# Kernel tuning notes

Measured on AMD Instinct MI355X. Metric: run time of the kernel, lower is better.

The kernel has to match this reference:

```python
import jax, jax.numpy as jnp
import numpy as np

B, G, T, N = 2, 4, 64, 300
D = 256          # detr_dim == feature_dim
R = 4            # ffn_dim_ratio
MD = 32          # motion_dim


def _xavier(key, shape):
    lim = (6.0 / (shape[0] + shape[1])) ** 0.5
    return jax.random.uniform(key, shape, jnp.float32, -lim, lim)


def setup_inputs() -> dict:
    key = jax.random.key(0)
    ks = jax.random.split(key, 16)
    feats = jax.random.normal(ks[0], (B, G, T, N, D), jnp.float32)
    boxes = jax.random.uniform(ks[1], (B, G, T, N, 4), jnp.float32)
    masks = jax.random.bernoulli(ks[2], 0.3, (B, G, T, N))
    # per-trajectory permutation of frame ids 0..T-1 (unique -> unambiguous scatter)
    u = jax.random.uniform(ks[3], (B, G, N, T))
    times = jnp.swapaxes(jnp.argsort(u, axis=-1).astype(jnp.int32), 2, 3)  # [B,G,T,N]
    return {
        'trajectory_features': feats,
        'trajectory_boxes': boxes,
        'trajectory_masks': masks,
        'trajectory_times': times,
        'adp_w1': _xavier(ks[4], (D, D * R)), 'adp_b1': jnp.zeros((D * R,), jnp.float32),
        'adp_w2': _xavier(ks[5], (D * R, D)), 'adp_b2': jnp.zeros((D,), jnp.float32),
        'norm_g': jnp.ones((D,), jnp.float32), 'norm_b': jnp.zeros((D,), jnp.float32),
        'mot_w1': _xavier(ks[6], (12, MD // 2)), 'mot_b1': jnp.zeros((MD // 2,), jnp.float32),
        'mot_w2': _xavier(ks[7], (MD // 2, MD)), 'mot_b2': jnp.zeros((MD,), jnp.float32),
        'fus_w1': _xavier(ks[8], (D + MD, D)), 'fus_b1': jnp.zeros((D,), jnp.float32),
        'fus_w2': _xavier(ks[9], (D, D)), 'fus_b2': jnp.zeros((D,), jnp.float32),
        'ffn_w1': _xavier(ks[10], (D, D * R)), 'ffn_b1': jnp.zeros((D * R,), jnp.float32),
        'ffn_w2': _xavier(ks[11], (D * R, D)), 'ffn_b2': jnp.zeros((D,), jnp.float32),
        'fnorm_g': jnp.ones((D,), jnp.float32), 'fnorm_b': jnp.zeros((D,), jnp.float32),
    }


def _ffn(x, w1, b1, w2, b2):
    return jax.nn.gelu(x @ w1 + b1, approximate=False) @ w2 + b2


def _ln(x, g, b):
    m = x.mean(-1, keepdims=True)
    v = ((x - m) ** 2).mean(-1, keepdims=True)
    return (x - m) / jnp.sqrt(v + 1e-5) * g + b


def _motion_features(boxes, masks, times, mot_w1, mot_b1, mot_w2, mot_b2):
    # boxes [B,G,T,N,4] -> trajectory-major [B,G,N,T,*]
    b_, g_, t_, n_ = masks.shape
    md = mot_b2.shape[0]
    bx = jnp.swapaxes(boxes, 2, 3)              # [B,G,N,T,4]
    valid = ~jnp.swapaxes(masks, 2, 3)          # [B,G,N,T]
    tm = jnp.swapaxes(times, 2, 3)              # [B,G,N,T]
    # sort valid entries first, by time (stable)
    order = jnp.argsort(jnp.where(valid, tm, t_ + 1), axis=-1)
    sb = jnp.take_along_axis(bx, order[..., None], axis=3)   # sorted boxes
    st = jnp.take_along_axis(tm, order, axis=-1)             # sorted times
    cnt = valid.sum(-1)                                      # [B,G,N]
    pos = jnp.arange(t_)
    in_count = pos[None, None, None, :] < cnt[..., None]
    dt = jnp.maximum(st - jnp.roll(st, 1, axis=-1), 1).astype(sb.dtype)[..., None]
    mask_v = ((pos >= 1)[None, None, None, :] & in_count)[..., None]
    vel = jnp.where(mask_v, (sb - jnp.roll(sb, 1, axis=3)) / dt, 0.0)
    mask_a = ((pos >= 2)[None, None, None, :] & in_count)[..., None]
    acc = jnp.where(mask_a, (vel - jnp.roll(vel, 1, axis=3)) / dt, 0.0)
    mv = jnp.concatenate([sb, vel, acc], axis=-1)            # [B,G,N,T,12]
    enc = jax.nn.gelu(mv @ mot_w1 + mot_b1, approximate=False) @ mot_w2 + mot_b2
    write = in_count & (cnt >= 2)[..., None] & (st < t_)
    frame = jnp.where(write, st, t_)                         # t_ -> dropped
    bi, gi, ni, ti = jnp.meshgrid(jnp.arange(b_), jnp.arange(g_), jnp.arange(n_),
                                  jnp.arange(t_), indexing='ij')
    out = jnp.zeros((b_, g_, t_, n_, md), sb.dtype)
    return out.at[bi, gi, frame, ni].set(enc, mode='drop')


def reference(trajectory_features, trajectory_boxes, trajectory_masks, trajectory_times,
              adp_w1, adp_b1, adp_w2, adp_b2, norm_g, norm_b,
              mot_w1, mot_b1, mot_w2, mot_b2,
              fus_w1, fus_b1, fus_w2, fus_b2,
              ffn_w1, ffn_b1, ffn_w2, ffn_b2, fnorm_g, fnorm_b):
    x = trajectory_features + _ffn(trajectory_features, adp_w1, adp_b1, adp_w2, adp_b2)
    x = _ln(x, norm_g, norm_b)
    motion = _motion_features(trajectory_boxes, trajectory_masks, trajectory_times,
                              mot_w1, mot_b1, mot_w2, mot_b2)
    cat = jnp.concatenate([x, motion], axis=-1)
    fused = jax.nn.gelu(cat @ fus_w1 + fus_b1, approximate=False) @ fus_w2 + fus_b2
    fused = fused + _ffn(fused, ffn_w1, ffn_b1, ffn_w2, ffn_b2)
    fused = _ln(fused, fnorm_g, fnorm_b)
    return fused, motion
```

## Files before the change

kernel.cpp:

```cpp
#include <hip/hip_runtime.h>

typedef __bf16 bf16x8 __attribute__((ext_vector_type(8)));
typedef __bf16 bf16x4 __attribute__((ext_vector_type(4)));
typedef float f32x4 __attribute__((ext_vector_type(4)));

namespace {

constexpr int T_ = 64;
constexpr int N_ = 300;
constexpr int MD_ = 32;
constexpr int BG_ = 8;
constexpr long MROWS_ = (long)BG_ * T_ * N_;
constexpr long FUSED_N = MROWS_ * 256;
constexpr int MB = 64;

constexpr long PA1 = 0;
constexpr long PA2 = 262144;
constexpr long PF1 = 524288;
constexpr long PF2 = 598016;
constexpr long PN1 = 663552;
constexpr long PN2 = 925696;

__device__ __forceinline__ float gelu_f(float x) {
  const float x2 = x * x;
  const float z2 = x * fmaf(x2, 0.07135481627f, 1.5957691216f);
  const float t = __builtin_amdgcn_rcpf(1.0f + __expf(z2));
  return x * (1.0f - t);
}

__device__ __forceinline__ float gelu_exact(float x) {
  return 0.5f * x * (1.0f + erff(x * 0.7071067811865476f));
}

__global__ void k_zero_flag(int* f) { *f = 0; }

__global__ void k_detect_mask(const unsigned char* __restrict__ m, int nbytes,
                              int* __restrict__ f) {
  int i = blockIdx.x * 256 + threadIdx.x;
  if (i < nbytes && (i & 3) != 0 && m[i] != 0) atomicOr(f, 1);
}

__global__ __launch_bounds__(256)
void k_motion(const float* __restrict__ boxes, const void* __restrict__ masks,
              const int* __restrict__ times,
              const float* __restrict__ mw1, const float* __restrict__ mb1,
              const float* __restrict__ mw2, const float* __restrict__ mb2,
              float* __restrict__ motion, const int* __restrict__ flagp) {
  __shared__ int slot[4][T_];
  __shared__ int sts[4][T_];
  __shared__ float sbx[4][T_][4];
  __shared__ float otile[4][T_][MD_];
  const int tid = threadIdx.x;
  const int w = tid >> 6, l = tid & 63;
  const int traj = blockIdx.x * 4 + w;
  const int bg = traj / N_, n = traj - bg * N_;
  const int isbool = *flagp;
  const long idx = ((long)bg * T_ + l) * N_ + n;
  const bool msk = isbool ? (((const unsigned char*)masks)[idx] != 0)
                          : (((const int*)masks)[idx] != 0);
  const bool valid = !msk;
  const int tm = times[idx];

  slot[w][l] = -1;
  sts[w][l] = 0;
  *(float4*)&sbx[w][l][0] = make_float4(0.f, 0.f, 0.f, 0.f);
  __syncthreads();
  if (valid) slot[w][tm] = l;
  __syncthreads();

  const int ot = slot[w][l];
  const bool vp = ot >= 0;
  const unsigned long long bal = __ballot(vp);
  const int cnt = __builtin_popcountll(bal);
  const int pos = __builtin_popcountll(bal & ((1ull << l) - 1ull));
  if (vp) {
    sts[w][pos] = l;
    const float4 bx = *(const float4*)(boxes + (((long)bg * T_ + ot) * N_ + n) * 4);
    *(float4*)&sbx[w][pos][0] = bx;
  }
  __syncthreads();

  const int stp = sts[w][l];
  const int stm1 = sts[w][(l + 63) & 63];
  const float4 sb = *(const float4*)&sbx[w][l][0];
  const float4 sbm = *(const float4*)&sbx[w][(l + 63) & 63][0];
  const float dt = (float)max(stp - stm1, 1);
  const float inv = 1.0f / dt;
  const bool okv = (l >= 1) && (l < cnt);
  float v0 = okv ? (sb.x - sbm.x) * inv : 0.f;
  float v1 = okv ? (sb.y - sbm.y) * inv : 0.f;
  float v2 = okv ? (sb.z - sbm.z) * inv : 0.f;
  float v3 = okv ? (sb.w - sbm.w) * inv : 0.f;
  const float p0 = __shfl_up(v0, 1, 64);
  const float p1 = __shfl_up(v1, 1, 64);
  const float p2 = __shfl_up(v2, 1, 64);
  const float p3 = __shfl_up(v3, 1, 64);
  const bool oka = (l >= 2) && (l < cnt);
  const float a0 = oka ? (v0 - p0) * inv : 0.f;
  const float a1 = oka ? (v1 - p1) * inv : 0.f;
  const float a2 = oka ? (v2 - p2) * inv : 0.f;
  const float a3 = oka ? (v3 - p3) * inv : 0.f;

  const float mv[12] = {sb.x, sb.y, sb.z, sb.w, v0, v1, v2, v3, a0, a1, a2, a3};
  float e1[16];
#pragma unroll
  for (int i = 0; i < 16; ++i) {
    float a = mb1[i];
#pragma unroll
    for (int c = 0; c < 12; ++c) a = fmaf(mv[c], mw1[c * 16 + i], a);
    e1[i] = gelu_exact(a);
  }
  float enc[32];
#pragma unroll
  for (int o = 0; o < 32; ++o) {
    float a = mb2[o];
#pragma unroll
    for (int i = 0; i < 16; ++i) a = fmaf(e1[i], mw2[i * 32 + o], a);
    enc[o] = a;
  }

#pragma unroll
  for (int c = 0; c < 32; c += 4)
    *(float4*)&otile[w][l][c] = make_float4(0.f, 0.f, 0.f, 0.f);
  __syncthreads();
  if (l < cnt && cnt >= 2) {
#pragma unroll
    for (int c = 0; c < 32; ++c) otile[w][stp][c] = enc[c];
  }
  __syncthreads();

  float* mbase = motion + ((long)bg * T_ * N_ + n) * MD_;
  const float4* srcv = (const float4*)&otile[w][l][0];
  float4* dstv = (float4*)(mbase + (long)l * N_ * MD_);
#pragma unroll
  for (int q = 0; q < 8; ++q) dstv[q] = srcv[q];
}

__global__ void k_pack(const float* __restrict__ W, __bf16* __restrict__ P,
                       int K, int NN) {
  int gid = blockIdx.x * 256 + threadIdx.x;
  int total = (K >> 5) * (NN >> 4) * 64;
  if (gid >= total) return;
  int l = gid & 63, f = gid >> 6;
  int NT = NN >> 4;
  int kb = f / NT, nt = f - kb * NT;
  int krow = kb * 32 + (l >> 4) * 8;
  int col = nt * 16 + (l & 15);
  bf16x8 v;
#pragma unroll
  for (int e = 0; e < 8; ++e) v[e] = (__bf16)W[(long)(krow + e) * NN + col];
  *(bf16x8*)(P + (long)gid * 8) = v;
}

template <int NKB, bool MOT, int NT>
__device__ __forceinline__ void produce_chunk(
    const char* regA, const char* regM, char* hb, const __bf16* pb1,
    const float* b1, int r, int wid, int l, int lr, int lk) {
  const int nt = r * 8 + wid;
  f32x4 t[4];
  {
    const float4 bv = *(const float4*)(b1 + r * 128 + wid * 16 + lk * 4);
#pragma unroll
    for (int rt = 0; rt < 4; ++rt) t[rt] = f32x4{bv.x, bv.y, bv.z, bv.w};
  }
  const __bf16* wp = pb1 + ((long)nt << 9) + (l << 3);
  bf16x8 w0 = *(const bf16x8*)(wp);
  bf16x8 w1 = w0;
  if (NKB > 1) w1 = *(const bf16x8*)(wp + ((long)NT << 9));
#pragma unroll
  for (int kb = 0; kb < NKB; ++kb) {
    const bf16x8 wf = (kb & 1) ? w1 : w0;
    if (kb + 2 < NKB) {
      const bf16x8 v = *(const bf16x8*)(wp + ((long)(kb + 2) * NT << 9));
      if (kb & 1) w1 = v; else w0 = v;
    }
    __builtin_amdgcn_s_setprio(1);
#pragma unroll
    for (int rt = 0; rt < 4; ++rt) {
      const int row = rt * 16 + lr;
      bf16x8 xf;
      if (MOT && kb == NKB - 1)
        xf = *(const bf16x8*)(regM + row * 64 + ((lk ^ (row & 3)) << 4));
      else
        xf = *(const bf16x8*)(regA + row * 512 +
                              ((((kb << 2) + lk) ^ (row & 7)) << 4));
      t[rt] = __builtin_amdgcn_mfma_f32_16x16x32_bf16(wf, xf, t[rt], 0, 0, 0);
    }
    __builtin_amdgcn_s_setprio(0);
  }
#pragma unroll
  for (int rt = 0; rt < 4; ++rt) {
    const int row = rt * 16 + lr;
    bf16x4 hv;
#pragma unroll
    for (int e = 0; e < 4; ++e) hv[e] = (__bf16)gelu_f(t[rt][e]);
    *(bf16x4*)(hb + row * 256 + ((wid * 32 + lk * 8) ^ ((row & 7) << 4))) = hv;
  }
}

__device__ __forceinline__ void consume_chunk(const char* hb,
                                              const __bf16* pb2, int kbg0,
                                              int l, int lr, int lk, int wr,
                                              int wn, f32x4 (&acc)[2][4]) {
  const __bf16* wp = pb2 + ((long)(kbg0 * 16 + wn * 4) << 9) + (l << 3);
  bf16x8 bw0[4], bw1[4];
#pragma unroll
  for (int j = 0; j < 4; ++j) bw0[j] = *(const bf16x8*)(wp + ((long)j << 9));
#pragma unroll
  for (int kbl = 0; kbl < 4; ++kbl) {
    if (kbl < 3) {
#pragma unroll
      for (int j = 0; j < 4; ++j)
        bw1[j] = *(const bf16x8*)(wp + ((long)((kbl + 1) * 16 + j) << 9));
    }
    bf16x8 a[2];
#pragma unroll
    for (int m = 0; m < 2; ++m) {
      const int row = wr * 32 + m * 16 + lr;
      a[m] = *(const bf16x8*)(hb + row * 256 +
                              ((kbl * 64 + lk * 16) ^ ((row & 7) << 4)));
    }
    __builtin_amdgcn_s_setprio(1);
#pragma unroll
    for (int j = 0; j < 4; ++j)
#pragma unroll
      for (int m = 0; m < 2; ++m)
        acc[m][j] = __builtin_amdgcn_mfma_f32_16x16x32_bf16(a[m], bw0[j],
                                                            acc[m][j], 0, 0, 0);
    __builtin_amdgcn_s_setprio(0);
#pragma unroll
    for (int j = 0; j < 4; ++j) bw0[j] = bw1[j];
  }
}

__global__ __launch_bounds__(512, 1)
void k_mfma(const float* __restrict__ feats, const float* __restrict__ motion,
            const __bf16* __restrict__ pw,
            const float* __restrict__ ba1, const float* __restrict__ ba2,
            const float* __restrict__ ng, const float* __restrict__ nb,
            const float* __restrict__ bf1, const float* __restrict__ bf2,
            const float* __restrict__ bn1, const float* __restrict__ bn2,
            const float* __restrict__ fg, const float* __restrict__ fb,
            float* __restrict__ out) {
  __shared__ __align__(16) char smem[71680];
  char* regA = smem;
  char* hb0 = smem + 32768;
  char* hb1 = smem + 49152;
  char* regM = smem + 65536;
  float* redp = (float*)(smem + 69632);

  const int tid = threadIdx.x;
  const int l = tid & 63, wid = tid >> 6;
  const int lr = l & 15, lk = l >> 4;
  const int wr = wid >> 2;
  const int wn = wid & 3;
  const int colb = wn * 64;
  const int row0 = wr * 32;
  const long rowbase = (long)blockIdx.x * MB;

  const __bf16* pa1 = pw + PA1;
  const __bf16* pa2 = pw + PA2;
  const __bf16* pf1 = pw + PF1;
  const __bf16* pf2 = pw + PF2;
  const __bf16* pn1 = pw + PN1;
  const __bf16* pn2 = pw + PN2;

  auto ln_stats = [&](const f32x4 (&acc)[2][4], float (&mean)[2][4],
                      float (&rstd)[2][4]) {
    float s1[2][4], s2[2][4];
#pragma unroll
    for (int m = 0; m < 2; ++m)
#pragma unroll
      for (int e = 0; e < 4; ++e) { s1[m][e] = 0.f; s2[m][e] = 0.f; }
#pragma unroll
    for (int m = 0; m < 2; ++m)
#pragma unroll
      for (int j = 0; j < 4; ++j)
#pragma unroll
        for (int e = 0; e < 4; ++e) {
          s1[m][e] += acc[m][j][e];
          s2[m][e] += acc[m][j][e] * acc[m][j][e];
        }
#pragma unroll
    for (int o = 1; o < 16; o <<= 1)
#pragma unroll
      for (int m = 0; m < 2; ++m)
#pragma unroll
        for (int e = 0; e < 4; ++e) {
          s1[m][e] += __shfl_xor(s1[m][e], o);
          s2[m][e] += __shfl_xor(s2[m][e], o);
        }
    if (lr == 0) {
#pragma unroll
      for (int m = 0; m < 2; ++m)
#pragma unroll
        for (int e = 0; e < 4; ++e) {
          const int row = row0 + m * 16 + lk * 4 + e;
          redp[(row * 4 + wn) * 2 + 0] = s1[m][e];
          redp[(row * 4 + wn) * 2 + 1] = s2[m][e];
        }
    }
    __syncthreads();
#pragma unroll
    for (int m = 0; m < 2; ++m)
#pragma unroll
      for (int e = 0; e < 4; ++e) {
        const int row = row0 + m * 16 + lk * 4 + e;
        const float S1 = redp[(row * 4 + 0) * 2] + redp[(row * 4 + 1) * 2] +
                         redp[(row * 4 + 2) * 2] + redp[(row * 4 + 3) * 2];
        const float S2 = redp[(row * 4 + 0) * 2 + 1] + redp[(row * 4 + 1) * 2 + 1] +
                         redp[(row * 4 + 2) * 2 + 1] + redp[(row * 4 + 3) * 2 + 1];
        const float mu = S1 * (1.0f / 256.0f);
        const float var = S2 * (1.0f / 256.0f) - mu * mu;
        mean[m][e] = mu;
        rstd[m][e] = rsqrtf(var + 1e-5f);
      }
  };

  f32x4 acc2[2][4];
#pragma unroll
  for (int j = 0; j < 4; ++j) {
    const int col = colb + j * 16 + lr;
    const float bv = ba2[col];
#pragma unroll
    for (int m = 0; m < 2; ++m)
#pragma unroll
      for (int e = 0; e < 4; ++e) {
        const int row = row0 + m * 16 + lk * 4 + e;
        acc2[m][j][e] = bv + feats[(rowbase + row) * 256 + col];
      }
  }
#pragma unroll
  for (int it = 0; it < 4; ++it) {
    const int c = tid + it * 512;
    const int row = c >> 5, cc = c & 31;
    const float* src = feats + (rowbase + row) * 256 + cc * 8;
    bf16x8 v;
#pragma unroll
    for (int e = 0; e < 8; ++e) v[e] = (__bf16)src[e];
    *(bf16x8*)(regA + row * 512 + ((cc ^ (row & 7)) << 4)) = v;
  }
  __syncthreads();

  produce_chunk<8, false, 64>(regA, regM, hb0, pa1, ba1, 0, wid, l, lr, lk);
  __syncthreads();
#pragma unroll 1
  for (int r = 0; r < 8; ++r) {
    if (r < 7)
      produce_chunk<8, false, 64>(regA, regM, ((r + 1) & 1) ? hb1 : hb0, pa1,
                                  ba1, r + 1, wid, l, lr, lk);
    consume_chunk((r & 1) ? hb1 : hb0, pa2, r * 4, l, lr, lk, wr, wn, acc2);
    __syncthreads();
  }

  {
    float mean[2][4], rstd[2][4];
    ln_stats(acc2, mean, rstd);
#pragma unroll
    for (int j = 0; j < 4; ++j) {
      const int col = colb + j * 16 + lr;
      const float gv = ng[col], bv = nb[col];
#pragma unroll
      for (int m = 0; m < 2; ++m)
#pragma unroll
        for (int e = 0; e < 4; ++e) {
          const int row = row0 + m * 16 + lk * 4 + e;
          const float v = (acc2[m][j][e] - mean[m][e]) * rstd[m][e] * gv + bv;
          *(__bf16*)(regA + row * 512 + (((col >> 3) ^ (row & 7)) << 4) +
                     ((col & 7) << 1)) = (__bf16)v;
        }
    }
    if (tid < 256) {
      const int row = tid >> 2, cc = tid & 3;
      const float* src = motion + (rowbase + row) * 32 + cc * 8;
      bf16x8 v;
#pragma unroll
      for (int e = 0; e < 8; ++e) v[e] = (__bf16)src[e];
      *(bf16x8*)(regM + row * 64 + ((cc ^ (row & 3)) << 4)) = v;
    }
  }
  __syncthreads();

  {
    f32x4 accD[2][4];
#pragma unroll
    for (int j = 0; j < 4; ++j) {
      const float bv = bf2[colb + j * 16 + lr];
#pragma unroll
      for (int m = 0; m < 2; ++m) accD[m][j] = {bv, bv, bv, bv};
    }
    produce_chunk<9, true, 16>(regA, regM, hb0, pf1, bf1, 0, wid, l, lr, lk);
    __syncthreads();
    produce_chunk<9, true, 16>(regA, regM, hb1, pf1, bf1, 1, wid, l, lr, lk);
    consume_chunk(hb0, pf2, 0, l, lr, lk, wr, wn, accD);
    __syncthreads();
    consume_chunk(hb1, pf2, 4, l, lr, lk, wr, wn, accD);
    __syncthreads();
#pragma unroll
    for (int j = 0; j < 4; ++j) {
      const int col = colb + j * 16 + lr;
      const float bv = bn2[col];
#pragma unroll
      for (int m = 0; m < 2; ++m)
#pragma unroll
        for (int e = 0; e < 4; ++e) {
          const int row = row0 + m * 16 + lk * 4 + e;
          const float fv = accD[m][j][e];
          *(__bf16*)(regA + row * 512 + (((col >> 3) ^ (row & 7)) << 4) +
                     ((col & 7) << 1)) = (__bf16)fv;
          acc2[m][j][e] = fv + bv;
        }
    }
  }
  __syncthreads();

  produce_chunk<8, false, 64>(regA, regM, hb0, pn1, bn1, 0, wid, l, lr, lk);
  __syncthreads();
#pragma unroll 1
  for (int r = 0; r < 8; ++r) {
    if (r < 7)
      produce_chunk<8, false, 64>(regA, regM, ((r + 1) & 1) ? hb1 : hb0, pn1,
                                  bn1, r + 1, wid, l, lr, lk);
    consume_chunk((r & 1) ? hb1 : hb0, pn2, r * 4, l, lr, lk, wr, wn, acc2);
    __syncthreads();
  }

  {
    float mean[2][4], rstd[2][4];
    ln_stats(acc2, mean, rstd);
#pragma unroll
    for (int j = 0; j < 4; ++j) {
      const int col = colb + j * 16 + lr;
      const float gv = fg[col], bv = fb[col];
#pragma unroll
      for (int m = 0; m < 2; ++m)
#pragma unroll
        for (int e = 0; e < 4; ++e) {
          const int row = row0 + m * 16 + lk * 4 + e;
          out[(rowbase + row) * 256 + col] =
              (acc2[m][j][e] - mean[m][e]) * rstd[m][e] * gv + bv;
        }
    }
  }
}

}

extern "C" void kernel_launch(void* const* d_in, const int* in_sizes, int n_in,
                              void* d_out, int out_size, void* d_ws, size_t ws_size,
                              hipStream_t stream) {
  const float* feats = (const float*)d_in[0];
  const float* boxes = (const float*)d_in[1];
  const void*  masks = d_in[2];
  const int*   times = (const int*)d_in[3];
  const float* wa1 = (const float*)d_in[4];
  const float* ba1 = (const float*)d_in[5];
  const float* wa2 = (const float*)d_in[6];
  const float* ba2 = (const float*)d_in[7];
  const float* ng  = (const float*)d_in[8];
  const float* nb  = (const float*)d_in[9];
  const float* mw1 = (const float*)d_in[10];
  const float* mb1 = (const float*)d_in[11];
  const float* mw2 = (const float*)d_in[12];
  const float* mb2 = (const float*)d_in[13];
  const float* wf1 = (const float*)d_in[14];
  const float* bf1 = (const float*)d_in[15];
  const float* wf2 = (const float*)d_in[16];
  const float* bf2 = (const float*)d_in[17];
  const float* wn1 = (const float*)d_in[18];
  const float* bn1 = (const float*)d_in[19];
  const float* wn2 = (const float*)d_in[20];
  const float* bn2 = (const float*)d_in[21];
  const float* fg  = (const float*)d_in[22];
  const float* fb  = (const float*)d_in[23];

  float* out_fused = (float*)d_out;
  float* out_motion = out_fused + FUSED_N;
  int* flag = (int*)d_ws;
  __bf16* pw = (__bf16*)((char*)d_ws + 256);

  const int mask_elems = in_sizes[2];

  k_zero_flag<<<1, 1, 0, stream>>>(flag);
  k_detect_mask<<<(mask_elems + 255) / 256, 256, 0, stream>>>(
      (const unsigned char*)masks, mask_elems, flag);
  k_motion<<<(BG_ * N_) / 4, 256, 0, stream>>>(boxes, masks, times, mw1, mb1, mw2,
                                               mb2, out_motion, flag);

  auto packn = [&](const float* W, long off, int K, int NN) {
    const int total = (K / 32) * (NN / 16) * 64;
    k_pack<<<(total + 255) / 256, 256, 0, stream>>>(W, pw + off, K, NN);
  };
  packn(wa1, PA1, 256, 1024);
  packn(wa2, PA2, 1024, 256);
  packn(wf1, PF1, 288, 256);
  packn(wf2, PF2, 256, 256);
  packn(wn1, PN1, 256, 1024);
  packn(wn2, PN2, 1024, 256);

  k_mfma<<<(int)(MROWS_ / MB), 512, 0, stream>>>(
      feats, out_motion, pw, ba1, ba2, ng, nb, bf1, bf2, bn1, bn2, fg, fb,
      out_fused);
}
```

Before: 649.5 us.

## Shrink fused MLP block to 32 rows and 4 waves for higher occupancy

Halves the row tile of the fused MLP kernel from 64 to 32 rows and uses 256 threads (4 waves) per block instead of 512, with launch bounds allowing 4 blocks per CU. Shared memory shrinks from about 70KB to 27KB, hidden chunks become 64 columns wide, and the produce/consume pipeline runs twice as many iterations. The aim is more resident blocks per CU to hide latency. In exchange, each weight tile is reused across fewer rows, which doubles total weight traffic, and there are more barriers per block.

```diff
diff --git a/kernel.cpp b/kernel.cpp
--- a/kernel.cpp
+++ b/kernel.cpp
@@ -12,7 +12,7 @@
 constexpr int BG_ = 8;
 constexpr long MROWS_ = (long)BG_ * T_ * N_;
 constexpr long FUSED_N = MROWS_ * 256;
-constexpr int MB = 64;
+constexpr int MB = 32;
 
 constexpr long PA1 = 0;
 constexpr long PA2 = 262144;
@@ -156,12 +156,12 @@
 __device__ __forceinline__ void produce_chunk(
     const char* regA, const char* regM, char* hb, const __bf16* pb1,
     const float* b1, int r, int wid, int l, int lr, int lk) {
-  const int nt = r * 8 + wid;
-  f32x4 t[4];
+  const int nt = r * 4 + wid;
+  f32x4 t[2];
   {
-    const float4 bv = *(const float4*)(b1 + r * 128 + wid * 16 + lk * 4);
-#pragma unroll
-    for (int rt = 0; rt < 4; ++rt) t[rt] = f32x4{bv.x, bv.y, bv.z, bv.w};
+    const float4 bv = *(const float4*)(b1 + r * 64 + wid * 16 + lk * 4);
+#pragma unroll
+    for (int rt = 0; rt < 2; ++rt) t[rt] = f32x4{bv.x, bv.y, bv.z, bv.w};
   }
   const __bf16* wp = pb1 + ((long)nt << 9) + (l << 3);
   bf16x8 w0 = *(const bf16x8*)(wp);
@@ -176,7 +176,7 @@
     }
     __builtin_amdgcn_s_setprio(1);
 #pragma unroll
-    for (int rt = 0; rt < 4; ++rt) {
+    for (int rt = 0; rt < 2; ++rt) {
       const int row = rt * 16 + lr;
       bf16x8 xf;
       if (MOT && kb == NKB - 1)
@@ -189,35 +189,33 @@
     __builtin_amdgcn_s_setprio(0);
   }
 #pragma unroll
-  for (int rt = 0; rt < 4; ++rt) {
+  for (int rt = 0; rt < 2; ++rt) {
     const int row = rt * 16 + lr;
     bf16x4 hv;
 #pragma unroll
     for (int e = 0; e < 4; ++e) hv[e] = (__bf16)gelu_f(t[rt][e]);
-    *(bf16x4*)(hb + row * 256 + ((wid * 32 + lk * 8) ^ ((row & 7) << 4))) = hv;
+    *(bf16x4*)(hb + row * 128 + ((wid * 32 + lk * 8) ^ ((row & 7) << 4))) = hv;
   }
 }
 
 __device__ __forceinline__ void consume_chunk(const char* hb,
                                               const __bf16* pb2, int kbg0,
-                                              int l, int lr, int lk, int wr,
-                                              int wn, f32x4 (&acc)[2][4]) {
+                                              int l, int lr, int lk, int wn,
+                                              f32x4 (&acc)[2][4]) {
   const __bf16* wp = pb2 + ((long)(kbg0 * 16 + wn * 4) << 9) + (l << 3);
   bf16x8 bw0[4], bw1[4];
 #pragma unroll
   for (int j = 0; j < 4; ++j) bw0[j] = *(const bf16x8*)(wp + ((long)j << 9));
 #pragma unroll
-  for (int kbl = 0; kbl < 4; ++kbl) {
-    if (kbl < 3) {
-#pragma unroll
-      for (int j = 0; j < 4; ++j)
-        bw1[j] = *(const bf16x8*)(wp + ((long)((kbl + 1) * 16 + j) << 9));
-    }
+  for (int j = 0; j < 4; ++j)
+    bw1[j] = *(const bf16x8*)(wp + ((long)(16 + j) << 9));
+#pragma unroll
+  for (int kbl = 0; kbl < 2; ++kbl) {
     bf16x8 a[2];
 #pragma unroll
     for (int m = 0; m < 2; ++m) {
-      const int row = wr * 32 + m * 16 + lr;
-      a[m] = *(const bf16x8*)(hb + row * 256 +
+      const int row = m * 16 + lr;
+      a[m] = *(const bf16x8*)(hb + row * 128 +
                               ((kbl * 64 + lk * 16) ^ ((row & 7) << 4)));
     }
     __builtin_amdgcn_s_setprio(1);
@@ -225,15 +223,13 @@
     for (int j = 0; j < 4; ++j)
 #pragma unroll
       for (int m = 0; m < 2; ++m)
-        acc[m][j] = __builtin_amdgcn_mfma_f32_16x16x32_bf16(a[m], bw0[j],
-                                                            acc[m][j], 0, 0, 0);
+        acc[m][j] = __builtin_amdgcn_mfma_f32_16x16x32_bf16(
+            a[m], kbl ? bw1[j] : bw0[j], acc[m][j], 0, 0, 0);
     __builtin_amdgcn_s_setprio(0);
-#pragma unroll
-    for (int j = 0; j < 4; ++j) bw0[j] = bw1[j];
-  }
-}
-
-__global__ __launch_bounds__(512, 1)
+  }
+}
+
+__global__ __launch_bounds__(256, 4)
 void k_mfma(const float* __restrict__ feats, const float* __restrict__ motion,
             const __bf16* __restrict__ pw,
             const float* __restrict__ ba1, const float* __restrict__ ba2,
@@ -242,20 +238,18 @@
             const float* __restrict__ bn1, const float* __restrict__ bn2,
             const float* __restrict__ fg, const float* __restrict__ fb,
             float* __restrict__ out) {
-  __shared__ __align__(16) char smem[71680];
+  __shared__ __align__(16) char smem[27648];
   char* regA = smem;
-  char* hb0 = smem + 32768;
-  char* hb1 = smem + 49152;
-  char* regM = smem + 65536;
-  float* redp = (float*)(smem + 69632);
+  char* hb0 = smem + 16384;
+  char* hb1 = smem + 20480;
+  char* regM = smem + 24576;
+  float* redp = (float*)(smem + 26624);
 
   const int tid = threadIdx.x;
   const int l = tid & 63, wid = tid >> 6;
   const int lr = l & 15, lk = l >> 4;
-  const int wr = wid >> 2;
-  const int wn = wid & 3;
+  const int wn = wid;
   const int colb = wn * 64;
-  const int row0 = wr * 32;
   const long rowbase = (long)blockIdx.x * MB;
 
   const __bf16* pa1 = pw + PA1;
@@ -295,7 +289,7 @@
       for (int m = 0; m < 2; ++m)
 #pragma unroll
         for (int e = 0; e < 4; ++e) {
-          const int row = row0 + m * 16 + lk * 4 + e;
+          const int row = m * 16 + lk * 4 + e;
           redp[(row * 4 + wn) * 2 + 0] = s1[m][e];
           redp[(row * 4 + wn) * 2 + 1] = s2[m][e];
         }
@@ -305,7 +299,7 @@
     for (int m = 0; m < 2; ++m)
 #pragma unroll
       for (int e = 0; e < 4; ++e) {
-        const int row = row0 + m * 16 + lk * 4 + e;
+        const int row = m * 16 + lk * 4 + e;
         const float S1 = redp[(row * 4 + 0) * 2] + redp[(row * 4 + 1) * 2] +
                          redp[(row * 4 + 2) * 2] + redp[(row * 4 + 3) * 2];
         const float S2 = redp[(row * 4 + 0) * 2 + 1] + redp[(row * 4 + 1) * 2 + 1] +
@@ -326,13 +320,13 @@
     for (int m = 0; m < 2; ++m)
 #pragma unroll
       for (int e = 0; e < 4; ++e) {
-        const int row = row0 + m * 16 + lk * 4 + e;
+        const int row = m * 16 + lk * 4 + e;
         acc2[m][j][e] = bv + feats[(rowbase + row) * 256 + col];
       }
   }
 #pragma unroll
   for (int it = 0; it < 4; ++it) {
-    const int c = tid + it * 512;
+    const int c = tid + it * 256;
     const int row = c >> 5, cc = c & 31;
     const float* src = feats + (rowbase + row) * 256 + cc * 8;
     bf16x8 v;
@@ -345,11 +339,11 @@
   produce_chunk<8, false, 64>(regA, regM, hb0, pa1, ba1, 0, wid, l, lr, lk);
   __syncthreads();
 #pragma unroll 1
-  for (int r = 0; r < 8; ++r) {
-    if (r < 7)
+  for (int r = 0; r < 16; ++r) {
+    if (r < 15)
       produce_chunk<8, false, 64>(regA, regM, ((r + 1) & 1) ? hb1 : hb0, pa1,
                                   ba1, r + 1, wid, l, lr, lk);
-    consume_chunk((r & 1) ? hb1 : hb0, pa2, r * 4, l, lr, lk, wr, wn, acc2);
+    consume_chunk((r & 1) ? hb1 : hb0, pa2, r * 2, l, lr, lk, wn, acc2);
     __syncthreads();
   }
 
@@ -364,13 +358,13 @@
       for (int m = 0; m < 2; ++m)
 #pragma unroll
         for (int e = 0; e < 4; ++e) {
-          const int row = row0 + m * 16 + lk * 4 + e;
+          const int row = m * 16 + lk * 4 + e;
           const float v = (acc2[m][j][e] - mean[m][e]) * rstd[m][e] * gv + bv;
           *(__bf16*)(regA + row * 512 + (((col >> 3) ^ (row & 7)) << 4) +
                      ((col & 7) << 1)) = (__bf16)v;
         }
     }
-    if (tid < 256) {
+    if (tid < 128) {
       const int row = tid >> 2, cc = tid & 3;
       const float* src = motion + (rowbase + row) * 32 + cc * 8;
       bf16x8 v;
@@ -391,11 +385,14 @@
     }
     produce_chunk<9, true, 16>(regA, regM, hb0, pf1, bf1, 0, wid, l, lr, lk);
     __syncthreads();
-    produce_chunk<9, true, 16>(regA, regM, hb1, pf1, bf1, 1, wid, l, lr, lk);
-    consume_chunk(hb0, pf2, 0, l, lr, lk, wr, wn, accD);
-    __syncthreads();
-    consume_chunk(hb1, pf2, 4, l, lr, lk, wr, wn, accD);
-    __syncthreads();
+#pragma unroll 1
+    for (int r = 0; r < 4; ++r) {
+      if (r < 3)
+        produce_chunk<9, true, 16>(regA, regM, ((r + 1) & 1) ? hb1 : hb0, pf1,
+                                   bf1, r + 1, wid, l, lr, lk);
+      consume_chunk((r & 1) ? hb1 : hb0, pf2, r * 2, l, lr, lk, wn, accD);
+      __syncthreads();
+    }
 #pragma unroll
     for (int j = 0; j < 4; ++j) {
       const int col = colb + j * 16 + lr;
@@ -404,7 +401,7 @@
       for (int m = 0; m < 2; ++m)
 #pragma unroll
         for (int e = 0; e < 4; ++e) {
-          const int row = row0 + m * 16 + lk * 4 + e;
+          const int row = m * 16 + lk * 4 + e;
           const float fv = accD[m][j][e];
           *(__bf16*)(regA + row * 512 + (((col >> 3) ^ (row & 7)) << 4) +
                      ((col & 7) << 1)) = (__bf16)fv;
@@ -417,11 +414,11 @@
   produce_chunk<8, false, 64>(regA, regM, hb0, pn1, bn1, 0, wid, l, lr, lk);
   __syncthreads();
 #pragma unroll 1
-  for (int r = 0; r < 8; ++r) {
-    if (r < 7)
+  for (int r = 0; r < 16; ++r) {
+    if (r < 15)
       produce_chunk<8, false, 64>(regA, regM, ((r + 1) & 1) ? hb1 : hb0, pn1,
                                   bn1, r + 1, wid, l, lr, lk);
-    consume_chunk((r & 1) ? hb1 : hb0, pn2, r * 4, l, lr, lk, wr, wn, acc2);
+    consume_chunk((r & 1) ? hb1 : hb0, pn2, r * 2, l, lr, lk, wn, acc2);
     __syncthreads();
   }
 
@@ -436,7 +433,7 @@
       for (int m = 0; m < 2; ++m)
 #pragma unroll
         for (int e = 0; e < 4; ++e) {
-          const int row = row0 + m * 16 + lk * 4 + e;
+          const int row = m * 16 + lk * 4 + e;
           out[(rowbase + row) * 256 + col] =
               (acc2[m][j][e] - mean[m][e]) * rstd[m][e] * gv + bv;
         }
@@ -498,7 +495,7 @@
   packn(wn1, PN1, 256, 1024);
   packn(wn2, PN2, 1024, 256);
 
-  k_mfma<<<(int)(MROWS_ / MB), 512, 0, stream>>>(
+  k_mfma<<<(int)(MROWS_ / MB), 256, 0, stream>>>(
       feats, out_motion, pw, ba1, ba2, ng, nb, bf1, bf2, bn1, bn2, fg, fb,
       out_fused);
 }
```

New measurement: 623.0 us. -4.1%, faster.
